# Kernel tuning notes

Hardware: AMD Instinct MI355X
Metric: run time of the kernel (lower is better)

Reference implementation:

```python
import jax, jax.numpy as jnp
import numpy as np

SCALE = 32.0      # backbone feature->image coordinate scale (stride)
LOG_EPS = 1e-8    # geometry.safe_log epsilon


def _safe_log(x):
    return jnp.log(jnp.maximum(x, LOG_EPS))


def setup_inputs() -> dict:
    key = jax.random.key(0)
    k1, k2, k3, k4, k5, k6 = jax.random.split(key, 6)
    B, P, L = 128, 4096, 128
    cls_scores = jax.random.normal(k1, (B, 2 * P), dtype=jnp.float32)
    bbox_deltas = jax.random.normal(k2, (B, 4 * P), dtype=jnp.float32) * 0.1
    # RoI in feature coordinates: x,y in [0,40), w,h in [1,11)
    roi_xy = jax.random.uniform(k3, (B, P, 2), dtype=jnp.float32) * 40.0
    roi_wh = jax.random.uniform(k4, (B, P, 2), dtype=jnp.float32) * 10.0 + 1.0
    roi = jnp.concatenate([roi_xy, roi_wh], axis=-1)
    # Ground-truth labels in image coordinates: x,y in [0,1280), w,h in [32,352)
    lab_xy = jax.random.uniform(k5, (B, L, 2), dtype=jnp.float32) * 1280.0
    lab_wh = jax.random.uniform(k6, (B, L, 2), dtype=jnp.float32) * 320.0 + 32.0
    labels = jnp.concatenate([lab_xy, lab_wh], axis=-1)
    return {
        "cls_scores": cls_scores,
        "bbox_deltas": bbox_deltas,
        "roi": roi,
        "labels": labels,
        "neg_enabled": 1,
    }


def reference(cls_scores, bbox_deltas, roi, labels, neg_enabled):
    """Vectorized port of ClassifierModel._compute_loss summed over the batch.

    cls_scores  [B, 2P] laid out [class, proposal] (cls[i::P] -> per-proposal logits)
    bbox_deltas [B, 4P] laid out [coord, proposal]
    roi         [B, P, 4] proposals in feature coords (x,y,w,h)
    labels      [B, L, 4] ground-truth boxes in image coords (x,y,w,h)
    """
    B, P = roi.shape[0], roi.shape[1]
    roi_img = roi.astype(jnp.float32) * SCALE  # feature -> image coords

    # --- IoU matrix [B, L, P] (geometry.calculate_IoU over all label/proposal pairs)
    l = labels[:, :, None, :]   # [B, L, 1, 4]
    r = roi_img[:, None, :, :]  # [B, 1, P, 4]
    ix = jnp.maximum(0.0, jnp.minimum(l[..., 0] + l[..., 2], r[..., 0] + r[..., 2]) - jnp.maximum(l[..., 0], r[..., 0]))
    iy = jnp.maximum(0.0, jnp.minimum(l[..., 1] + l[..., 3], r[..., 1] + r[..., 3]) - jnp.maximum(l[..., 1], r[..., 1]))
    inter = ix * iy
    union = l[..., 2] * l[..., 3] + r[..., 2] * r[..., 3] - inter
    iou = jnp.where(union > 0.0, inter / union, 0.0)  # [B, L, P]

    # --- matching: argmax over labels where any IoU is nonzero, else -1
    any_hit = jnp.sum((iou != 0.0).astype(jnp.int32), axis=1) > 0        # [B, P]
    match = jnp.where(any_hit, jnp.argmax(iou, axis=1), -1)              # [B, P]
    pos = match > 0  # NOTE: original uses match[i] > 0 (strict), kept faithfully

    matched = jnp.take_along_axis(labels, jnp.clip(match, 0)[:, :, None], axis=1)  # [B, P, 4]
    tx = (matched[..., 0] - roi_img[..., 0]) / roi_img[..., 2]
    ty = (matched[..., 1] - roi_img[..., 1]) / roi_img[..., 3]
    tw = _safe_log(matched[..., 2] / roi_img[..., 2])
    th = _safe_log(matched[..., 3] / roi_img[..., 3])
    targets = jnp.stack([tx, ty, tw, th], axis=-1)                        # [B, P, 4]
    preds = bbox_deltas.reshape(B, 4, P).transpose(0, 2, 1)               # [B, P, 4]

    # Huber (delta=1, mean over the 4 coords) per proposal
    err = targets - preds
    ae = jnp.abs(err)
    huber = jnp.mean(jnp.where(ae <= 1.0, 0.5 * err * err, ae - 0.5), axis=-1)  # [B, P]

    # --- classification: softmax over the two per-proposal logits, then
    # CategoricalCrossentropy(probs, const) = -sum(probs * log(const))
    logits = cls_scores.reshape(B, 2, P).transpose(0, 2, 1)               # [B, P, 2]
    probs = jax.nn.softmax(logits, axis=-1)
    log_pos = jnp.log(jnp.array([0.1, 0.9], dtype=jnp.float32))
    log_neg = jnp.log(jnp.array([0.9, 0.1], dtype=jnp.float32))
    ce_pos = -jnp.sum(probs * log_pos, axis=-1)                           # [B, P]
    ce_neg = -jnp.sum(probs * log_neg, axis=-1)                           # [B, P]

    neg_term = jnp.where(jnp.asarray(neg_enabled) > 0, ce_neg, 0.0)
    per_prop = jnp.where(pos, 2.0 * huber + ce_pos, neg_term)             # [B, P]
    return jnp.sum(per_prop)
```

## Files before the change

### kernel.cpp

```cpp
#include <hip/hip_runtime.h>
#include <hip/hip_bf16.h>
#include <math.h>

#define BB 128
#define PP 4096
#define LL 128
#define BLOCK 256
#define CHUNKS (PP / BLOCK)
#define SCALE 32.0f

__global__ void zero_out_kernel(float* out) { out[0] = 0.0f; }

__global__ __launch_bounds__(BLOCK) void classifier_loss_kernel(
    const float* __restrict__ cls,
    const float* __restrict__ bbox,
    const float* __restrict__ roi,
    const float* __restrict__ labels,
    const int* __restrict__ neg_enabled,
    float* __restrict__ out)
{
    __shared__ float s_lab[LL][4];
    __shared__ float s_ext[LL][4];
    __shared__ float s_red[BLOCK / 64];

    const int b     = blockIdx.x / CHUNKS;
    const int chunk = blockIdx.x % CHUNKS;
    const int p     = chunk * BLOCK + threadIdx.x;

    if (threadIdx.x < LL) {
        const float* lp = labels + ((size_t)b * LL + threadIdx.x) * 4;
        float lx = lp[0], ly = lp[1], lw = lp[2], lh = lp[3];
        s_lab[threadIdx.x][0] = lx;
        s_lab[threadIdx.x][1] = ly;
        s_lab[threadIdx.x][2] = lw;
        s_lab[threadIdx.x][3] = lh;
        s_ext[threadIdx.x][0] = lx + lw;
        s_ext[threadIdx.x][1] = ly + lh;
        s_ext[threadIdx.x][2] = lw * lh;
        s_ext[threadIdx.x][3] = 0.0f;
    }
    __syncthreads();

    const float* rp = roi + ((size_t)b * PP + p) * 4;
    const float rx = rp[0] * SCALE, ry = rp[1] * SCALE;
    const float rw = rp[2] * SCALE, rh = rp[3] * SCALE;
    const float rx2 = rx + rw, ry2 = ry + rh;
    const float rarea = rw * rh;

    float best_inter, best_union;
    int   best_idx = 0;
    {
        float ix = fmaxf(0.0f, fminf(s_ext[0][0], rx2) - fmaxf(s_lab[0][0], rx));
        float iy = fmaxf(0.0f, fminf(s_ext[0][1], ry2) - fmaxf(s_lab[0][1], ry));
        best_inter = ix * iy;
        best_union = s_ext[0][2] + rarea - best_inter;
    }
    #pragma unroll 4
    for (int li = 1; li < LL; ++li) {
        float ix = fmaxf(0.0f, fminf(s_ext[li][0], rx2) - fmaxf(s_lab[li][0], rx));
        float iy = fmaxf(0.0f, fminf(s_ext[li][1], ry2) - fmaxf(s_lab[li][1], ry));
        float inter = ix * iy;
        float uni   = s_ext[li][2] + rarea - inter;
        bool gt = inter * best_union > best_inter * uni;
        best_inter = gt ? inter : best_inter;
        best_union = gt ? uni   : best_union;
        best_idx   = gt ? li    : best_idx;
    }

    const bool any_hit = best_inter > 0.0f;
    const bool pos     = any_hit && (best_idx > 0);

    const float s0 = cls[(size_t)b * 2 * PP + p];
    const float s1 = cls[(size_t)b * 2 * PP + PP + p];
    const float mx = fmaxf(s0, s1);
    const float e0 = expf(s0 - mx);
    const float e1 = expf(s1 - mx);
    const float inv = 1.0f / (e0 + e1);
    const float p0 = e0 * inv, p1 = e1 * inv;
    const float LOG01 = -2.3025850929940457f;
    const float LOG09 = -0.10536051565782628f;
    const float ce_pos = -(p0 * LOG01 + p1 * LOG09);
    const float ce_neg = -(p0 * LOG09 + p1 * LOG01);

    float per;
    if (pos) {
        float mxl = s_lab[best_idx][0];
        float myl = s_lab[best_idx][1];
        float mwl = s_lab[best_idx][2];
        float mhl = s_lab[best_idx][3];
        float tx = (mxl - rx) / rw;
        float ty = (myl - ry) / rh;
        float tw = logf(fmaxf(mwl / rw, 1e-8f));
        float th = logf(fmaxf(mhl / rh, 1e-8f));
        const float* bp = bbox + (size_t)b * 4 * PP + p;
        float px = bp[0];
        float py = bp[PP];
        float pw = bp[2 * PP];
        float ph = bp[3 * PP];
        float ex = tx - px, ey = ty - py, ew = tw - pw, eh = th - ph;
        float ax = fabsf(ex), ay = fabsf(ey), aw = fabsf(ew), ah = fabsf(eh);
        float hx = (ax <= 1.0f) ? 0.5f * ex * ex : ax - 0.5f;
        float hy = (ay <= 1.0f) ? 0.5f * ey * ey : ay - 0.5f;
        float hw = (aw <= 1.0f) ? 0.5f * ew * ew : aw - 0.5f;
        float hh = (ah <= 1.0f) ? 0.5f * eh * eh : ah - 0.5f;
        float huber = 0.25f * (hx + hy + hw + hh);
        per = 2.0f * huber + ce_pos;
    } else {
        per = (neg_enabled[0] > 0) ? ce_neg : 0.0f;
    }

    float v = per;
    #pragma unroll
    for (int off = 32; off > 0; off >>= 1)
        v += __shfl_down(v, off, 64);
    if ((threadIdx.x & 63) == 0)
        s_red[threadIdx.x >> 6] = v;
    __syncthreads();
    if (threadIdx.x == 0) {
        float blk = s_red[0] + s_red[1] + s_red[2] + s_red[3];
        atomicAdd(out, blk);
    }
}

extern "C" void kernel_launch(void* const* d_in, const int* in_sizes, int n_in,
                              void* d_out, int out_size, void* d_ws, size_t ws_size,
                              hipStream_t stream) {
    const float* cls    = (const float*)d_in[0];
    const float* bbox   = (const float*)d_in[1];
    const float* roi    = (const float*)d_in[2];
    const float* labels = (const float*)d_in[3];
    const int*   neg    = (const int*)d_in[4];
    float* out = (float*)d_out;

    zero_out_kernel<<<1, 1, 0, stream>>>(out);
    classifier_loss_kernel<<<dim3(BB * CHUNKS), dim3(BLOCK), 0, stream>>>(
        cls, bbox, roi, labels, neg, out);
}
```

Measured before the change: 109.3 us.

## Process two proposals per thread and read labels directly from global memory

```diff
diff --git a/kernel.cpp b/kernel.cpp
--- a/kernel.cpp
+++ b/kernel.cpp
@@ -6,10 +6,9 @@
 #define PP 4096
 #define LL 128
 #define BLOCK 256
-#define CHUNKS (PP / BLOCK)
+#define PROPS 2
+#define CHUNKS (PP / (BLOCK * PROPS))
 #define SCALE 32.0f
-
-__global__ void zero_out_kernel(float* out) { out[0] = 0.0f; }
 
 __global__ __launch_bounds__(BLOCK) void classifier_loss_kernel(
     const float* __restrict__ cls,
@@ -19,97 +18,104 @@
     const int* __restrict__ neg_enabled,
     float* __restrict__ out)
 {
-    __shared__ float s_lab[LL][4];
-    __shared__ float s_ext[LL][4];
     __shared__ float s_red[BLOCK / 64];
 
-    const int b     = blockIdx.x / CHUNKS;
-    const int chunk = blockIdx.x % CHUNKS;
-    const int p     = chunk * BLOCK + threadIdx.x;
+    const int b     = blockIdx.x >> 3;
+    const int chunk = blockIdx.x & (CHUNKS - 1);
+    const int pbase = chunk * (BLOCK * PROPS) + threadIdx.x;
 
-    if (threadIdx.x < LL) {
-        const float* lp = labels + ((size_t)b * LL + threadIdx.x) * 4;
-        float lx = lp[0], ly = lp[1], lw = lp[2], lh = lp[3];
-        s_lab[threadIdx.x][0] = lx;
-        s_lab[threadIdx.x][1] = ly;
-        s_lab[threadIdx.x][2] = lw;
-        s_lab[threadIdx.x][3] = lh;
-        s_ext[threadIdx.x][0] = lx + lw;
-        s_ext[threadIdx.x][1] = ly + lh;
-        s_ext[threadIdx.x][2] = lw * lh;
-        s_ext[threadIdx.x][3] = 0.0f;
-    }
-    __syncthreads();
+    const float* __restrict__ lab = labels + (size_t)b * LL * 4;
 
-    const float* rp = roi + ((size_t)b * PP + p) * 4;
-    const float rx = rp[0] * SCALE, ry = rp[1] * SCALE;
-    const float rw = rp[2] * SCALE, rh = rp[3] * SCALE;
-    const float rx2 = rx + rw, ry2 = ry + rh;
-    const float rarea = rw * rh;
+    float rx[PROPS], ry[PROPS], rx2[PROPS], ry2[PROPS], rarea[PROPS];
+    float bi[PROPS], bd[PROPS];
+    int   bidx[PROPS];
 
-    float best_inter, best_union;
-    int   best_idx = 0;
-    {
-        float ix = fmaxf(0.0f, fminf(s_ext[0][0], rx2) - fmaxf(s_lab[0][0], rx));
-        float iy = fmaxf(0.0f, fminf(s_ext[0][1], ry2) - fmaxf(s_lab[0][1], ry));
-        best_inter = ix * iy;
-        best_union = s_ext[0][2] + rarea - best_inter;
-    }
-    #pragma unroll 4
-    for (int li = 1; li < LL; ++li) {
-        float ix = fmaxf(0.0f, fminf(s_ext[li][0], rx2) - fmaxf(s_lab[li][0], rx));
-        float iy = fmaxf(0.0f, fminf(s_ext[li][1], ry2) - fmaxf(s_lab[li][1], ry));
-        float inter = ix * iy;
-        float uni   = s_ext[li][2] + rarea - inter;
-        bool gt = inter * best_union > best_inter * uni;
-        best_inter = gt ? inter : best_inter;
-        best_union = gt ? uni   : best_union;
-        best_idx   = gt ? li    : best_idx;
+    #pragma unroll
+    for (int j = 0; j < PROPS; ++j) {
+        const int p = pbase + j * BLOCK;
+        const float* rp = roi + ((size_t)b * PP + p) * 4;
+        rx[j]  = rp[0] * SCALE;
+        ry[j]  = rp[1] * SCALE;
+        float rw = rp[2] * SCALE, rh = rp[3] * SCALE;
+        rx2[j] = rx[j] + rw;
+        ry2[j] = ry[j] + rh;
+        rarea[j] = rw * rh;
+        bi[j] = -1.0f;
+        bd[j] = 1.0f;
+        bidx[j] = 0;
     }
 
-    const bool any_hit = best_inter > 0.0f;
-    const bool pos     = any_hit && (best_idx > 0);
+    #pragma unroll 4
+    for (int li = 0; li < LL; ++li) {
+        const float lx = lab[li * 4 + 0];
+        const float ly = lab[li * 4 + 1];
+        const float lw = lab[li * 4 + 2];
+        const float lh = lab[li * 4 + 3];
+        const float x2 = lx + lw;
+        const float y2 = ly + lh;
+        const float area = lw * lh;
+        #pragma unroll
+        for (int j = 0; j < PROPS; ++j) {
+            float ix = fmaxf(0.0f, fminf(x2, rx2[j]) - fmaxf(lx, rx[j]));
+            float iy = fmaxf(0.0f, fminf(y2, ry2[j]) - fmaxf(ly, ry[j]));
+            float inter = ix * iy;
+            float denom = area + rarea[j];
+            bool gt = inter * bd[j] > bi[j] * denom;
+            bi[j]   = gt ? inter : bi[j];
+            bd[j]   = gt ? denom : bd[j];
+            bidx[j] = gt ? li    : bidx[j];
+        }
+    }
 
-    const float s0 = cls[(size_t)b * 2 * PP + p];
-    const float s1 = cls[(size_t)b * 2 * PP + PP + p];
-    const float mx = fmaxf(s0, s1);
-    const float e0 = expf(s0 - mx);
-    const float e1 = expf(s1 - mx);
-    const float inv = 1.0f / (e0 + e1);
-    const float p0 = e0 * inv, p1 = e1 * inv;
     const float LOG01 = -2.3025850929940457f;
     const float LOG09 = -0.10536051565782628f;
-    const float ce_pos = -(p0 * LOG01 + p1 * LOG09);
-    const float ce_neg = -(p0 * LOG09 + p1 * LOG01);
+    const bool neg_on = neg_enabled[0] > 0;
 
-    float per;
-    if (pos) {
-        float mxl = s_lab[best_idx][0];
-        float myl = s_lab[best_idx][1];
-        float mwl = s_lab[best_idx][2];
-        float mhl = s_lab[best_idx][3];
-        float tx = (mxl - rx) / rw;
-        float ty = (myl - ry) / rh;
-        float tw = logf(fmaxf(mwl / rw, 1e-8f));
-        float th = logf(fmaxf(mhl / rh, 1e-8f));
-        const float* bp = bbox + (size_t)b * 4 * PP + p;
-        float px = bp[0];
-        float py = bp[PP];
-        float pw = bp[2 * PP];
-        float ph = bp[3 * PP];
-        float ex = tx - px, ey = ty - py, ew = tw - pw, eh = th - ph;
-        float ax = fabsf(ex), ay = fabsf(ey), aw = fabsf(ew), ah = fabsf(eh);
-        float hx = (ax <= 1.0f) ? 0.5f * ex * ex : ax - 0.5f;
-        float hy = (ay <= 1.0f) ? 0.5f * ey * ey : ay - 0.5f;
-        float hw = (aw <= 1.0f) ? 0.5f * ew * ew : aw - 0.5f;
-        float hh = (ah <= 1.0f) ? 0.5f * eh * eh : ah - 0.5f;
-        float huber = 0.25f * (hx + hy + hw + hh);
-        per = 2.0f * huber + ce_pos;
-    } else {
-        per = (neg_enabled[0] > 0) ? ce_neg : 0.0f;
+    float acc = 0.0f;
+    #pragma unroll
+    for (int j = 0; j < PROPS; ++j) {
+        const int p = pbase + j * BLOCK;
+        const bool pos = (bi[j] > 0.0f) && (bidx[j] > 0);
+
+        const float s0 = cls[(size_t)b * 2 * PP + p];
+        const float s1 = cls[(size_t)b * 2 * PP + PP + p];
+        const float mx = fmaxf(s0, s1);
+        const float e0 = expf(s0 - mx);
+        const float e1 = expf(s1 - mx);
+        const float inv = 1.0f / (e0 + e1);
+        const float p0 = e0 * inv, p1 = e1 * inv;
+        const float ce_pos = -(p0 * LOG01 + p1 * LOG09);
+        const float ce_neg = -(p0 * LOG09 + p1 * LOG01);
+
+        float per;
+        if (pos) {
+            const float* mp = lab + bidx[j] * 4;
+            float mxl = mp[0], myl = mp[1], mwl = mp[2], mhl = mp[3];
+            float rw = rx2[j] - rx[j];
+            float rh = ry2[j] - ry[j];
+            float tx = (mxl - rx[j]) / rw;
+            float ty = (myl - ry[j]) / rh;
+            float tw = logf(fmaxf(mwl / rw, 1e-8f));
+            float th = logf(fmaxf(mhl / rh, 1e-8f));
+            const float* bp = bbox + (size_t)b * 4 * PP + p;
+            float ex = tx - bp[0];
+            float ey = ty - bp[PP];
+            float ew = tw - bp[2 * PP];
+            float eh = th - bp[3 * PP];
+            float ax = fabsf(ex), ay = fabsf(ey), aw = fabsf(ew), ah = fabsf(eh);
+            float hx = (ax <= 1.0f) ? 0.5f * ex * ex : ax - 0.5f;
+            float hy = (ay <= 1.0f) ? 0.5f * ey * ey : ay - 0.5f;
+            float hw = (aw <= 1.0f) ? 0.5f * ew * ew : aw - 0.5f;
+            float hh = (ah <= 1.0f) ? 0.5f * eh * eh : ah - 0.5f;
+            float huber = 0.25f * (hx + hy + hw + hh);
+            per = 2.0f * huber + ce_pos;
+        } else {
+            per = neg_on ? ce_neg : 0.0f;
+        }
+        acc += per;
     }
 
-    float v = per;
+    float v = acc;
     #pragma unroll
     for (int off = 32; off > 0; off >>= 1)
         v += __shfl_down(v, off, 64);
@@ -132,7 +138,7 @@
     const int*   neg    = (const int*)d_in[4];
     float* out = (float*)d_out;
 
-    zero_out_kernel<<<1, 1, 0, stream>>>(out);
+    hipMemsetAsync(out, 0, sizeof(float) * out_size, stream);
     classifier_loss_kernel<<<dim3(BB * CHUNKS), dim3(BLOCK), 0, stream>>>(
         cls, bbox, roi, labels, neg, out);
 }
```

After: 115.4 us. 1.06x slower.

## Read labels via uniform global loads and simplify IoU argmax comparison

Applied to the files above, without the earlier changes.

```diff
diff --git a/kernel.cpp b/kernel.cpp
--- a/kernel.cpp
+++ b/kernel.cpp
@@ -8,8 +8,7 @@
 #define BLOCK 256
 #define CHUNKS (PP / BLOCK)
 #define SCALE 32.0f
-
-__global__ void zero_out_kernel(float* out) { out[0] = 0.0f; }
+#define LCHUNK 8
 
 __global__ __launch_bounds__(BLOCK) void classifier_loss_kernel(
     const float* __restrict__ cls,
@@ -19,27 +18,13 @@
     const int* __restrict__ neg_enabled,
     float* __restrict__ out)
 {
-    __shared__ float s_lab[LL][4];
-    __shared__ float s_ext[LL][4];
     __shared__ float s_red[BLOCK / 64];
 
-    const int b     = blockIdx.x / CHUNKS;
-    const int chunk = blockIdx.x % CHUNKS;
+    const int b     = blockIdx.x >> 4;
+    const int chunk = blockIdx.x & (CHUNKS - 1);
     const int p     = chunk * BLOCK + threadIdx.x;
 
-    if (threadIdx.x < LL) {
-        const float* lp = labels + ((size_t)b * LL + threadIdx.x) * 4;
-        float lx = lp[0], ly = lp[1], lw = lp[2], lh = lp[3];
-        s_lab[threadIdx.x][0] = lx;
-        s_lab[threadIdx.x][1] = ly;
-        s_lab[threadIdx.x][2] = lw;
-        s_lab[threadIdx.x][3] = lh;
-        s_ext[threadIdx.x][0] = lx + lw;
-        s_ext[threadIdx.x][1] = ly + lh;
-        s_ext[threadIdx.x][2] = lw * lh;
-        s_ext[threadIdx.x][3] = 0.0f;
-    }
-    __syncthreads();
+    const float* __restrict__ lab = labels + (size_t)b * LL * 4;
 
     const float* rp = roi + ((size_t)b * PP + p) * 4;
     const float rx = rp[0] * SCALE, ry = rp[1] * SCALE;
@@ -47,28 +32,36 @@
     const float rx2 = rx + rw, ry2 = ry + rh;
     const float rarea = rw * rh;
 
-    float best_inter, best_union;
+    float best_inter = -1.0f, best_denom = 1.0f;
     int   best_idx = 0;
-    {
-        float ix = fmaxf(0.0f, fminf(s_ext[0][0], rx2) - fmaxf(s_lab[0][0], rx));
-        float iy = fmaxf(0.0f, fminf(s_ext[0][1], ry2) - fmaxf(s_lab[0][1], ry));
-        best_inter = ix * iy;
-        best_union = s_ext[0][2] + rarea - best_inter;
-    }
-    #pragma unroll 4
-    for (int li = 1; li < LL; ++li) {
-        float ix = fmaxf(0.0f, fminf(s_ext[li][0], rx2) - fmaxf(s_lab[li][0], rx));
-        float iy = fmaxf(0.0f, fminf(s_ext[li][1], ry2) - fmaxf(s_lab[li][1], ry));
-        float inter = ix * iy;
-        float uni   = s_ext[li][2] + rarea - inter;
-        bool gt = inter * best_union > best_inter * uni;
-        best_inter = gt ? inter : best_inter;
-        best_union = gt ? uni   : best_union;
-        best_idx   = gt ? li    : best_idx;
+
+    for (int lc = 0; lc < LL; lc += LCHUNK) {
+        float lv[LCHUNK * 4];
+        #pragma unroll
+        for (int k = 0; k < LCHUNK * 4; ++k)
+            lv[k] = lab[lc * 4 + k];
+
+        #pragma unroll
+        for (int u = 0; u < LCHUNK; ++u) {
+            const float lx = lv[u * 4 + 0];
+            const float ly = lv[u * 4 + 1];
+            const float lw = lv[u * 4 + 2];
+            const float lh = lv[u * 4 + 3];
+            const float x2 = lx + lw;
+            const float y2 = ly + lh;
+            const float area = lw * lh;
+            float ix = fmaxf(0.0f, fminf(x2, rx2) - fmaxf(lx, rx));
+            float iy = fmaxf(0.0f, fminf(y2, ry2) - fmaxf(ly, ry));
+            float inter = ix * iy;
+            float denom = area + rarea;
+            bool gt = inter * best_denom > best_inter * denom;
+            best_inter = gt ? inter : best_inter;
+            best_denom = gt ? denom : best_denom;
+            best_idx   = gt ? (lc + u) : best_idx;
+        }
     }
 
-    const bool any_hit = best_inter > 0.0f;
-    const bool pos     = any_hit && (best_idx > 0);
+    const bool pos = (best_inter > 0.0f) && (best_idx > 0);
 
     const float s0 = cls[(size_t)b * 2 * PP + p];
     const float s1 = cls[(size_t)b * 2 * PP + PP + p];
@@ -84,20 +77,17 @@
 
     float per;
     if (pos) {
-        float mxl = s_lab[best_idx][0];
-        float myl = s_lab[best_idx][1];
-        float mwl = s_lab[best_idx][2];
-        float mhl = s_lab[best_idx][3];
+        const float* mp = lab + best_idx * 4;
+        float mxl = mp[0], myl = mp[1], mwl = mp[2], mhl = mp[3];
         float tx = (mxl - rx) / rw;
         float ty = (myl - ry) / rh;
         float tw = logf(fmaxf(mwl / rw, 1e-8f));
         float th = logf(fmaxf(mhl / rh, 1e-8f));
         const float* bp = bbox + (size_t)b * 4 * PP + p;
-        float px = bp[0];
-        float py = bp[PP];
-        float pw = bp[2 * PP];
-        float ph = bp[3 * PP];
-        float ex = tx - px, ey = ty - py, ew = tw - pw, eh = th - ph;
+        float ex = tx - bp[0];
+        float ey = ty - bp[PP];
+        float ew = tw - bp[2 * PP];
+        float eh = th - bp[3 * PP];
         float ax = fabsf(ex), ay = fabsf(ey), aw = fabsf(ew), ah = fabsf(eh);
         float hx = (ax <= 1.0f) ? 0.5f * ex * ex : ax - 0.5f;
         float hy = (ay <= 1.0f) ? 0.5f * ey * ey : ay - 0.5f;
@@ -132,7 +122,7 @@
     const int*   neg    = (const int*)d_in[4];
     float* out = (float*)d_out;
 
-    zero_out_kernel<<<1, 1, 0, stream>>>(out);
+    hipMemsetAsync(out, 0, sizeof(float) * out_size, stream);
     classifier_loss_kernel<<<dim3(BB * CHUNKS), dim3(BLOCK), 0, stream>>>(
         cls, bbox, roi, labels, neg, out);
 }
```

New measurement: 109.1 us. About the same (-0.2%).
